# Kernel optimization log

Measured on AMD Instinct MI355X. Metric: run time of the kernel, lower is better.

## Reference

```python
import jax, jax.numpy as jnp
import numpy as np

EPS = 1e-5


def spmm(rows, cols, vals, x):
    # x: (B, C, V); y[b,c,v] = sum_{e: rows[e]==v} vals[e] * x[b,c,cols[e]]
    B, C, V = x.shape
    xt = x.reshape(B * C, V).T                      # (V, B*C)
    msg = vals[:, None] * xt[cols]                  # (E, B*C)
    y = jax.ops.segment_sum(msg, rows, num_segments=V)
    return y.T.reshape(B, C, V)


def cheb_conv(x, W, b, rows, cols, vals):
    # W: (K, Cin, Cout); Chebyshev recurrence over node dim
    K = W.shape[0]
    Tk = [x]
    if K > 1:
        Tk.append(spmm(rows, cols, vals, x))
    for _ in range(2, K):
        Tk.append(2.0 * spmm(rows, cols, vals, Tk[-1]) - Tk[-2])
    T = jnp.stack(Tk)                               # (K, B, Cin, V)
    out = jnp.einsum('kbiv,kio->bov', T, W)
    if b is not None:
        out = out + b[None, :, None]
    return out


def bn(x, g, be):
    # BatchNorm1d training-mode stats over (batch, nodes) per channel
    m = jnp.mean(x, axis=(0, 2), keepdims=True)
    v = jnp.var(x, axis=(0, 2), keepdims=True)
    return (x - m) * jax.lax.rsqrt(v + EPS) * g[None, :, None] + be[None, :, None]


def res_block(x, rows, cols, vals, ga, bea, Wa, ba, gb, beb, Wb, bb, Ws=None):
    xn = bn(x, ga, bea)
    out = cheb_conv(xn, Wa, ba, rows, cols, vals)
    out = bn(jax.nn.relu(out), gb, beb)
    out = cheb_conv(out, Wb, bb, rows, cols, vals)
    sc = xn if Ws is None else cheb_conv(xn, Ws, None, rows, cols, vals)
    return jax.nn.relu(out + sc)


def setup_inputs() -> dict:
    key = jax.random.key(0)
    ks = iter(jax.random.split(key, 40))
    V, E, B, K = 50000, 800000, 8, 4
    d = {}
    d['x'] = jax.random.normal(next(ks), (B, 16, V), dtype=jnp.float32)
    d['lap_rows'] = jax.random.randint(next(ks), (E,), 0, V, dtype=jnp.int32)
    d['lap_cols'] = jax.random.randint(next(ks), (E,), 0, V, dtype=jnp.int32)
    d['lap_vals'] = jax.random.normal(next(ks), (E,), dtype=jnp.float32) * 0.05

    def w(shape, scale=0.1):
        return jax.random.normal(next(ks), shape, dtype=jnp.float32) * scale

    d['W_in'], d['b_in'] = w((K, 16, 32)), w((32,))
    # block 1: 32 -> [32] -> 32 (identity shortcut)
    d['g1a'], d['be1a'] = jnp.ones(32), jnp.zeros(32)
    d['W1a'], d['b1a'] = w((K, 32, 32)), w((32,))
    d['g1b'], d['be1b'] = jnp.ones(32), jnp.zeros(32)
    d['W1b'], d['b1b'] = w((K, 32, 32)), w((32,))
    # block 2: 32 -> [64] -> 64 (ChebConv K=1 shortcut, no bias)
    d['g2a'], d['be2a'] = jnp.ones(32), jnp.zeros(32)
    d['W2a'], d['b2a'] = w((K, 32, 64)), w((64,))
    d['g2b'], d['be2b'] = jnp.ones(64), jnp.zeros(64)
    d['W2b'], d['b2b'] = w((K, 64, 64)), w((64,))
    d['W2s'] = w((1, 32, 64))
    # block 3: 64 -> [64] -> 64 (identity shortcut)
    d['g3a'], d['be3a'] = jnp.ones(64), jnp.zeros(64)
    d['W3a'], d['b3a'] = w((K, 64, 64)), w((64,))
    d['g3b'], d['be3b'] = jnp.ones(64), jnp.zeros(64)
    d['W3b'], d['b3b'] = w((K, 64, 64)), w((64,))
    # output head
    d['g_out'], d['be_out'] = jnp.ones(64), jnp.zeros(64)
    d['W_out'], d['b_out'] = w((K, 64, 10)), w((10,))
    return d


def reference(x, lap_rows, lap_cols, lap_vals,
              W_in, b_in,
              g1a, be1a, W1a, b1a, g1b, be1b, W1b, b1b,
              g2a, be2a, W2a, b2a, g2b, be2b, W2b, b2b, W2s,
              g3a, be3a, W3a, b3a, g3b, be3b, W3b, b3b,
              g_out, be_out, W_out, b_out):
    r, c, v = lap_rows, lap_cols, lap_vals
    out = jax.nn.relu(cheb_conv(x, W_in, b_in, r, c, v))
    out = res_block(out, r, c, v, g1a, be1a, W1a, b1a, g1b, be1b, W1b, b1b)
    out = res_block(out, r, c, v, g2a, be2a, W2a, b2a, g2b, be2b, W2b, b2b, W2s)
    out = res_block(out, r, c, v, g3a, be3a, W3a, b3a, g3b, be3b, W3b, b3b)
    out = bn(out, g_out, be_out)
    out = jax.nn.relu(cheb_conv(out, W_out, b_out, r, c, v))
    pooled = jnp.max(out, axis=2)                   # global max pool over nodes -> (B, 10)
    return jax.nn.log_softmax(pooled, axis=1)
```

## Files before the change

### kernel.cpp

```cpp
#include <hip/hip_runtime.h>
#include <hip/hip_bf16.h>
#include <hip/hip_fp16.h>

__global__ void hist_kernel(const int* __restrict__ rows, int* __restrict__ counts, int E) {
    int i = blockIdx.x * blockDim.x + threadIdx.x;
    if (i < E) atomicAdd(&counts[rows[i]], 1);
}

__global__ void scan_kernel(const int* __restrict__ counts, int* __restrict__ row_ptr, int V) {
    __shared__ int wsum[4];
    __shared__ int s_carry;
    int t = threadIdx.x;
    int lane = t & 63, w = t >> 6;
    if (t == 0) { s_carry = 0; row_ptr[0] = 0; }
    __syncthreads();
    for (int base = 0; base < V; base += 256) {
        int i = base + t;
        int x = (i < V) ? counts[i] : 0;
        #pragma unroll
        for (int d = 1; d < 64; d <<= 1) {
            int y = __shfl_up(x, d);
            if (lane >= d) x += y;
        }
        if (lane == 63) wsum[w] = x;
        __syncthreads();
        int wo = 0;
        for (int j = 0; j < w; ++j) wo += wsum[j];
        int total = wsum[0] + wsum[1] + wsum[2] + wsum[3];
        if (i < V) row_ptr[i + 1] = s_carry + wo + x;
        __syncthreads();
        if (t == 0) s_carry += total;
        __syncthreads();
    }
}

__global__ void init_cursor_kernel(const int* __restrict__ row_ptr, int* __restrict__ cursor, int V) {
    int i = blockIdx.x * blockDim.x + threadIdx.x;
    if (i < V) cursor[i] = row_ptr[i];
}

__global__ void scatter_kernel(const int* __restrict__ rows, const int* __restrict__ cols,
                               const float* __restrict__ vals, int* __restrict__ cursor,
                               int* __restrict__ cols_s, float* __restrict__ vals_s, int E) {
    int i = blockIdx.x * blockDim.x + threadIdx.x;
    if (i < E) {
        int r = rows[i];
        int p = atomicAdd(&cursor[r], 1);
        cols_s[p] = cols[i];
        vals_s[p] = vals[i];
    }
}

__global__ void transpose_in_kernel(const float* __restrict__ x, __half* __restrict__ X, int V) {
    int total = V * 128;
    for (int i = blockIdx.x * blockDim.x + threadIdx.x; i < total; i += gridDim.x * blockDim.x) {
        int v = i >> 7;
        int t = i & 127;
        X[i] = __float2half(x[t * V + v]);
    }
}

template <int VPT> struct PackT;
template <> struct PackT<1> { using T = float;  };
template <> struct PackT<2> { using T = float2; };
template <> struct PackT<4> { using T = float4; };

template <int VPT>
__global__ __launch_bounds__(256) void spmm2_kernel(
    const int* __restrict__ row_ptr, const int* __restrict__ cols,
    const float* __restrict__ vals, const __half2* __restrict__ src,
    __half2* dst, const __half2* prev, int V) {
    using T = typename PackT<VPT>::T;
    union U { T raw; __half2 h[VPT]; };
    int lane = threadIdx.x & 63;
    int v = (blockIdx.x << 2) | (threadIdx.x >> 6);
    if (v >= V) return;
    const int W = VPT * 64;
    const size_t row = (size_t)v * W + lane * VPT;

    float pr[2 * VPT];
    bool hasp = (prev != nullptr);
    if (hasp) {
        U pv; pv.raw = *(const T*)(prev + row);
        #pragma unroll
        for (int j = 0; j < VPT; ++j) {
            float2 f = __half22float2(pv.h[j]);
            pr[2 * j] = f.x; pr[2 * j + 1] = f.y;
        }
    }
    float acc[2 * VPT];
    #pragma unroll
    for (int j = 0; j < 2 * VPT; ++j) acc[j] = 0.f;

    int e0 = row_ptr[v], e1 = row_ptr[v + 1];
    int e = e0;
    for (; e + 4 <= e1; e += 4) {
        int   c0 = cols[e],   c1 = cols[e + 1], c2 = cols[e + 2], c3 = cols[e + 3];
        float w0 = vals[e],   w1 = vals[e + 1], w2 = vals[e + 2], w3 = vals[e + 3];
        U g0, g1, g2, g3;
        g0.raw = *(const T*)(src + (size_t)c0 * W + lane * VPT);
        g1.raw = *(const T*)(src + (size_t)c1 * W + lane * VPT);
        g2.raw = *(const T*)(src + (size_t)c2 * W + lane * VPT);
        g3.raw = *(const T*)(src + (size_t)c3 * W + lane * VPT);
        #pragma unroll
        for (int j = 0; j < VPT; ++j) {
            float2 f;
            f = __half22float2(g0.h[j]); acc[2*j] += w0 * f.x; acc[2*j+1] += w0 * f.y;
            f = __half22float2(g1.h[j]); acc[2*j] += w1 * f.x; acc[2*j+1] += w1 * f.y;
            f = __half22float2(g2.h[j]); acc[2*j] += w2 * f.x; acc[2*j+1] += w2 * f.y;
            f = __half22float2(g3.h[j]); acc[2*j] += w3 * f.x; acc[2*j+1] += w3 * f.y;
        }
    }
    for (; e < e1; ++e) {
        int c = cols[e]; float wv = vals[e];
        U g; g.raw = *(const T*)(src + (size_t)c * W + lane * VPT);
        #pragma unroll
        for (int j = 0; j < VPT; ++j) {
            float2 f = __half22float2(g.h[j]);
            acc[2*j] += wv * f.x; acc[2*j+1] += wv * f.y;
        }
    }
    if (hasp) {
        #pragma unroll
        for (int j = 0; j < 2 * VPT; ++j) acc[j] = 2.f * acc[j] - pr[j];
    }
    U o;
    #pragma unroll
    for (int j = 0; j < VPT; ++j) o.h[j] = __floats2half2_rn(acc[2*j], acc[2*j+1]);
    *(T*)(dst + row) = o.raw;
}

__global__ __launch_bounds__(256) void mix2_kernel(
    const __half* __restrict__ in, int Cin, float* out, int Cout,
    const float* __restrict__ Wg, const float* __restrict__ bias,
    int accum, int V) {
    extern __shared__ float lds[];
    const int G  = 256 / Cout;
    const int NB = 4 * G;
    const int RS = 4 * Cin + 4;
    const int BCin = 8 * Cin, BCout = 8 * Cout;
    float* ins = lds;
    float* Ws  = lds + G * 8 * RS;

    int tid = threadIdx.x;
    int v0 = blockIdx.x * NB;

    for (int idx = tid; idx < (Cin * Cout) / 4; idx += 256)
        *(float4*)(Ws + idx * 4) = *(const float4*)(Wg + idx * 4);
    int total = NB * BCin;
    for (int idx = tid; idx * 2 < total; idx += 256) {
        int p = idx * 2;
        int n = p / BCin, r = p - n * BCin;
        int vv = v0 + n;
        float2 f = make_float2(0.f, 0.f);
        if (vv < V) f = __half22float2(*(const __half2*)(in + (size_t)vv * BCin + r));
        int b = r / Cin, ci = r - b * Cin;
        int g = n >> 2, j = n & 3;
        float* base = ins + (g * 8 + b) * RS + j;
        base[ci * 4]       = f.x;
        base[(ci + 1) * 4] = f.y;
    }
    __syncthreads();

    int g   = tid / Cout;
    int u   = tid - g * Cout;
    int CO8 = Cout >> 3;
    int b   = u / CO8;
    int co0 = (u - b * CO8) * 8;

    float a[4][8];
    #pragma unroll
    for (int n = 0; n < 4; ++n)
        #pragma unroll
        for (int k = 0; k < 8; ++k) a[n][k] = 0.f;

    const float* ib = ins + (g * 8 + b) * RS;
    for (int ci = 0; ci < Cin; ++ci) {
        float4 x  = *(const float4*)(ib + ci * 4);
        float4 w0 = *(const float4*)(Ws + ci * Cout + co0);
        float4 w1 = *(const float4*)(Ws + ci * Cout + co0 + 4);
        float xv[4] = {x.x, x.y, x.z, x.w};
        float wv[8] = {w0.x, w0.y, w0.z, w0.w, w1.x, w1.y, w1.z, w1.w};
        #pragma unroll
        for (int n = 0; n < 4; ++n)
            #pragma unroll
            for (int k = 0; k < 8; ++k)
                a[n][k] = fmaf(xv[n], wv[k], a[n][k]);
    }

    float bb[8];
    #pragma unroll
    for (int k = 0; k < 8; ++k) bb[k] = bias ? bias[co0 + k] : 0.f;

    #pragma unroll
    for (int n = 0; n < 4; ++n) {
        int vv = v0 + g * 4 + n;
        if (vv < V) {
            size_t oo = (size_t)vv * BCout + b * Cout + co0;
            float4 r0 = make_float4(a[n][0] + bb[0], a[n][1] + bb[1],
                                    a[n][2] + bb[2], a[n][3] + bb[3]);
            float4 r1 = make_float4(a[n][4] + bb[4], a[n][5] + bb[5],
                                    a[n][6] + bb[6], a[n][7] + bb[7]);
            if (accum) {
                float4 o0 = *(const float4*)(out + oo);
                float4 o1 = *(const float4*)(out + oo + 4);
                r0.x += o0.x; r0.y += o0.y; r0.z += o0.z; r0.w += o0.w;
                r1.x += o1.x; r1.y += o1.y; r1.z += o1.z; r1.w += o1.w;
            }
            *(float4*)(out + oo)     = r0;
            *(float4*)(out + oo + 4) = r1;
        }
    }
}

__global__ __launch_bounds__(256) void mix_kernel(
    const __half* __restrict__ in, int Cin, float* out, int Cout,
    const float* __restrict__ W, const float* __restrict__ bias,
    int accum, int V) {
    const int NPB = 4;
    __shared__ float in_s[NPB * 512];
    int t = threadIdx.x;
    int v0 = blockIdx.x * NPB;
    int BCin = 8 * Cin, BCout = 8 * Cout;
    for (int idx = t; idx < NPB * BCin; idx += 256) {
        int n = idx / BCin, r = idx - n * BCin;
        int v = v0 + n;
        in_s[idx] = (v < V) ? __half2float(in[(size_t)v * BCin + r]) : 0.f;
    }
    __syncthreads();
    for (int o = t; o < BCout; o += 256) {
        int b = o / Cout, co = o - b * Cout;
        float bb = bias ? bias[co] : 0.f;
        float a[NPB] = {bb, bb, bb, bb};
        for (int ci = 0; ci < Cin; ++ci) {
            float wv = W[ci * Cout + co];
            #pragma unroll
            for (int n = 0; n < NPB; ++n)
                a[n] += in_s[n * BCin + b * Cin + ci] * wv;
        }
        #pragma unroll
        for (int n = 0; n < NPB; ++n) {
            int v = v0 + n;
            if (v < V) {
                size_t oi = (size_t)v * BCout + o;
                float r = a[n];
                if (accum) r += out[oi];
                out[oi] = r;
            }
        }
    }
}

__global__ void bn_stats_h_kernel(const __half* __restrict__ x, int C,
                                  float* __restrict__ sums, size_t N) {
    __shared__ float s_sum[256];
    __shared__ float s_sq[256];
    int t = threadIdx.x;
    size_t i0 = (size_t)blockIdx.x * 256 + t;
    size_t step = (size_t)gridDim.x * 256;
    float s = 0.f, q = 0.f;
    for (size_t i = i0; i < N; i += step) {
        float v = __half2float(x[i]);
        s += v; q += v * v;
    }
    s_sum[t] = s; s_sq[t] = q;
    __syncthreads();
    for (int st = 128; st >= C; st >>= 1) {
        if (t < st) { s_sum[t] += s_sum[t + st]; s_sq[t] += s_sq[t + st]; }
        __syncthreads();
    }
    if (t < C) {
        atomicAdd(&sums[t], s_sum[t]);
        atomicAdd(&sums[C + t], s_sq[t]);
    }
}

__global__ void bn_stats_f_kernel(const float* __restrict__ x, int C, int relu_in,
                                  float* __restrict__ sums, size_t N) {
    __shared__ float s_sum[256];
    __shared__ float s_sq[256];
    int t = threadIdx.x;
    size_t i0 = (size_t)blockIdx.x * 256 + t;
    size_t step = (size_t)gridDim.x * 256;
    float s = 0.f, q = 0.f;
    for (size_t i = i0; i < N; i += step) {
        float v = x[i];
        if (relu_in) v = fmaxf(v, 0.f);
        s += v; q += v * v;
    }
    s_sum[t] = s; s_sq[t] = q;
    __syncthreads();
    for (int st = 128; st >= C; st >>= 1) {
        if (t < st) { s_sum[t] += s_sum[t + st]; s_sq[t] += s_sq[t + st]; }
        __syncthreads();
    }
    if (t < C) {
        atomicAdd(&sums[t], s_sum[t]);
        atomicAdd(&sums[C + t], s_sq[t]);
    }
}

__global__ void bn_finalize_kernel(const float* __restrict__ sums, const float* __restrict__ g,
                                   const float* __restrict__ be, float* __restrict__ ss,
                                   int C, float invN) {
    int c = threadIdx.x;
    if (c < C) {
        float m = sums[c] * invN;
        float var = sums[C + c] * invN - m * m;
        float s = g[c] * rsqrtf(var + 1e-5f);
        ss[c] = s;
        ss[C + c] = be[c] - m * s;
    }
}

__global__ void affine_h_kernel(__half* x, const float* __restrict__ ss, int C, size_t N) {
    size_t stride = (size_t)gridDim.x * blockDim.x;
    for (size_t i = (size_t)blockIdx.x * blockDim.x + threadIdx.x; i < N; i += stride) {
        int c = (int)(i & (size_t)(C - 1));
        x[i] = __float2half(__half2float(x[i]) * ss[c] + ss[C + c]);
    }
}

__global__ void affine_f2h_kernel(const float* __restrict__ in, __half* __restrict__ out,
                                  const float* __restrict__ ss, int C, size_t N) {
    size_t stride = (size_t)gridDim.x * blockDim.x;
    for (size_t i = (size_t)blockIdx.x * blockDim.x + threadIdx.x; i < N; i += stride) {
        int c = (int)(i & (size_t)(C - 1));
        float v = fmaxf(in[i], 0.f);
        out[i] = __float2half(v * ss[c] + ss[C + c]);
    }
}

__global__ void store_relu_kernel(const float* __restrict__ acc, __half* x0,
                                  int add, size_t N) {
    size_t stride = (size_t)gridDim.x * blockDim.x;
    for (size_t i = (size_t)blockIdx.x * blockDim.x + threadIdx.x; i < N; i += stride) {
        float r = acc[i];
        if (add) r += __half2float(x0[i]);
        x0[i] = __float2half(fmaxf(r, 0.f));
    }
}

__global__ void maxpool_kernel(const float* __restrict__ x, float* __restrict__ pooled, int V) {
    __shared__ float red[256];
    int o = blockIdx.x;
    float m = 0.f;
    for (int v = threadIdx.x; v < V; v += 256)
        m = fmaxf(m, x[(size_t)v * 80 + o]);
    red[threadIdx.x] = m;
    __syncthreads();
    for (int st = 128; st > 0; st >>= 1) {
        if (threadIdx.x < st) red[threadIdx.x] = fmaxf(red[threadIdx.x], red[threadIdx.x + st]);
        __syncthreads();
    }
    if (threadIdx.x == 0) pooled[o] = red[0];
}

__global__ void lsm_kernel(const float* __restrict__ pooled, float* __restrict__ out) {
    int b = threadIdx.x;
    if (b < 8) {
        float m = -1e30f;
        for (int c = 0; c < 10; ++c) m = fmaxf(m, pooled[b * 10 + c]);
        float s = 0.f;
        for (int c = 0; c < 10; ++c) s += expf(pooled[b * 10 + c] - m);
        float l = logf(s);
        for (int c = 0; c < 10; ++c)
            out[b * 10 + c] = pooled[b * 10 + c] - m - l;
    }
}

__global__ void encode_kernel(float* out, float val) {
    int i = threadIdx.x;
    if (i < 80) out[i] = val;
}

extern "C" void kernel_launch(void* const* d_in, const int* in_sizes, int n_in,
                              void* d_out, int out_size, void* d_ws, size_t ws_size,
                              hipStream_t stream) {
    (void)in_sizes; (void)n_in; (void)out_size;
    const int V = 50000, E = 800000;

    auto al = [](size_t x) { return (x + 255) & ~(size_t)255; };
    const size_t ACCB = al((size_t)V * 512 * sizeof(float));
    const size_t FB   = al((size_t)V * 512 * sizeof(__half));
    const size_t need = ACCB + 3 * FB + al((V + 1) * 4) + al(V * 4) + al(E * 4) + al(E * 4)
                      + al(8 * 128 * 4) + al(8 * 128 * 4) + al(80 * 4);
    if (ws_size < need) {
        encode_kernel<<<1, 128, 0, stream>>>((float*)d_out, (float)(ws_size >> 20));
        return;
    }

    const float* x_in = (const float*)d_in[0];
    const int* rows   = (const int*)d_in[1];
    const int* colsi  = (const int*)d_in[2];
    const float* lvals = (const float*)d_in[3];
    const float* W_in = (const float*)d_in[4];
    const float* b_in = (const float*)d_in[5];
    const float* g1a = (const float*)d_in[6],  *be1a = (const float*)d_in[7];
    const float* W1a = (const float*)d_in[8],  *b1a  = (const float*)d_in[9];
    const float* g1b = (const float*)d_in[10], *be1b = (const float*)d_in[11];
    const float* W1b = (const float*)d_in[12], *b1b  = (const float*)d_in[13];
    const float* g2a = (const float*)d_in[14], *be2a = (const float*)d_in[15];
    const float* W2a = (const float*)d_in[16], *b2a  = (const float*)d_in[17];
    const float* g2b = (const float*)d_in[18], *be2b = (const float*)d_in[19];
    const float* W2b = (const float*)d_in[20], *b2b  = (const float*)d_in[21];
    const float* W2s = (const float*)d_in[22];
    const float* g3a = (const float*)d_in[23], *be3a = (const float*)d_in[24];
    const float* W3a = (const float*)d_in[25], *b3a  = (const float*)d_in[26];
    const float* g3b = (const float*)d_in[27], *be3b = (const float*)d_in[28];
    const float* W3b = (const float*)d_in[29], *b3b  = (const float*)d_in[30];
    const float* g_o = (const float*)d_in[31], *be_o = (const float*)d_in[32];
    const float* W_o = (const float*)d_in[33], *b_o  = (const float*)d_in[34];

    char* wp = (char*)d_ws;
    auto take = [&](size_t bytes) -> void* { void* p = (void*)wp; wp += al(bytes); return p; };
    float*  ACC = (float*)take((size_t)V * 512 * sizeof(float));
    __half* B0  = (__half*)take((size_t)V * 512 * sizeof(__half));
    __half* B1  = (__half*)take((size_t)V * 512 * sizeof(__half));
    __half* B2  = (__half*)take((size_t)V * 512 * sizeof(__half));
    int* row_ptr  = (int*)take((V + 1) * sizeof(int));
    int* cursor   = (int*)take(V * sizeof(int));
    int* cols_s   = (int*)take(E * sizeof(int));
    float* vals_s = (float*)take(E * sizeof(float));
    float* bn_sums = (float*)take(8 * 128 * sizeof(float));
    float* aff     = (float*)take(8 * 128 * sizeof(float));
    float* pooled  = (float*)take(80 * sizeof(float));

    hipMemsetAsync(cursor, 0, V * sizeof(int), stream);
    hipMemsetAsync(bn_sums, 0, 8 * 128 * sizeof(float), stream);
    hist_kernel<<<(E + 255) / 256, 256, 0, stream>>>(rows, cursor, E);
    scan_kernel<<<1, 256, 0, stream>>>(cursor, row_ptr, V);
    init_cursor_kernel<<<(V + 255) / 256, 256, 0, stream>>>(row_ptr, cursor, V);
    scatter_kernel<<<(E + 255) / 256, 256, 0, stream>>>(rows, colsi, lvals, cursor, cols_s, vals_s, E);
    transpose_in_kernel<<<4096, 256, 0, stream>>>(x_in, B0, V);

    auto spmm = [&](const __half* src, __half* dst, const __half* prev, int C) {
        int grid = (V + 3) / 4;
        if (C == 16)
            spmm2_kernel<1><<<grid, 256, 0, stream>>>(row_ptr, cols_s, vals_s,
                (const __half2*)src, (__half2*)dst, (const __half2*)prev, V);
        else if (C == 32)
            spmm2_kernel<2><<<grid, 256, 0, stream>>>(row_ptr, cols_s, vals_s,
                (const __half2*)src, (__half2*)dst, (const __half2*)prev, V);
        else
            spmm2_kernel<4><<<grid, 256, 0, stream>>>(row_ptr, cols_s, vals_s,
                (const __half2*)src, (__half2*)dst, (const __half2*)prev, V);
    };
    auto mix = [&](const __half* in, int Cin, int Cout, const float* W,
                   const float* bias, int accum) {
        if (Cout == 32 || Cout == 64) {
            int G = 256 / Cout, NB = 4 * G, RS = 4 * Cin + 4;
            size_t ldsb = (size_t)(G * 8 * RS + Cin * Cout) * sizeof(float);
            mix2_kernel<<<(V + NB - 1) / NB, 256, ldsb, stream>>>(in, Cin, ACC, Cout,
                                                                  W, bias, accum, V);
        } else {
            mix_kernel<<<(V + 3) / 4, 256, 0, stream>>>(in, Cin, ACC, Cout, W, bias, accum, V);
        }
    };
    auto stats_h = [&](const __half* xb, int C, int slot, const float* g, const float* be) {
        bn_stats_h_kernel<<<1024, 256, 0, stream>>>(xb, C, bn_sums + slot * 128, (size_t)V * 8 * C);
        bn_finalize_kernel<<<1, 64, 0, stream>>>(bn_sums + slot * 128, g, be, aff + slot * 128, C,
                                                 1.f / ((float)V * 8.f));
    };
    auto stats_f = [&](const float* xb, int C, int relu, int slot, const float* g, const float* be) {
        bn_stats_f_kernel<<<1024, 256, 0, stream>>>(xb, C, relu, bn_sums + slot * 128, (size_t)V * 8 * C);
        bn_finalize_kernel<<<1, 64, 0, stream>>>(bn_sums + slot * 128, g, be, aff + slot * 128, C,
                                                 1.f / ((float)V * 8.f));
    };
    auto affine_h = [&](__half* xb, int C, int slot) {
        affine_h_kernel<<<2048, 256, 0, stream>>>(xb, aff + slot * 128, C, (size_t)V * 8 * C);
    };
    auto affine_f2h = [&](const float* in, __half* out, int C, int slot) {
        affine_f2h_kernel<<<2048, 256, 0, stream>>>(in, out, aff + slot * 128, C, (size_t)V * 8 * C);
    };
    auto store_relu = [&](int add, int C) {
        store_relu_kernel<<<2048, 256, 0, stream>>>(ACC, B0, add, (size_t)V * 8 * C);
    };
    auto cheb_a = [&](int Cin, int Cout, const float* W, const float* bias) {
        mix(B0, Cin, Cout, W, bias, 0);
        spmm(B0, B1, nullptr, Cin);
        mix(B1, Cin, Cout, W + 1 * Cin * Cout, nullptr, 1);
        spmm(B1, B2, B0, Cin);
        mix(B2, Cin, Cout, W + 2 * Cin * Cout, nullptr, 1);
        spmm(B2, B1, B1, Cin);
        mix(B1, Cin, Cout, W + 3 * Cin * Cout, nullptr, 1);
    };
    auto cheb_b = [&](int C, const float* W, const float* bias) {
        mix(B1, C, C, W, bias, 0);
        spmm(B1, B2, nullptr, C);
        mix(B2, C, C, W + 1 * C * C, nullptr, 1);
        spmm(B2, B1, B1, C);
        mix(B1, C, C, W + 2 * C * C, nullptr, 1);
        spmm(B1, B2, B2, C);
        mix(B2, C, C, W + 3 * C * C, nullptr, 1);
    };

    cheb_a(16, 32, W_in, b_in);
    store_relu(0, 32);

    stats_h(B0, 32, 0, g1a, be1a);
    affine_h(B0, 32, 0);
    cheb_a(32, 32, W1a, b1a);
    stats_f(ACC, 32, 1, 1, g1b, be1b);
    affine_f2h(ACC, B1, 32, 1);
    cheb_b(32, W1b, b1b);
    store_relu(1, 32);

    stats_h(B0, 32, 2, g2a, be2a);
    affine_h(B0, 32, 2);
    cheb_a(32, 64, W2a, b2a);
    stats_f(ACC, 64, 1, 3, g2b, be2b);
    affine_f2h(ACC, B1, 64, 3);
    cheb_b(64, W2b, b2b);
    mix(B0, 32, 64, W2s, nullptr, 1);
    store_relu(0, 64);

    stats_h(B0, 64, 4, g3a, be3a);
    affine_h(B0, 64, 4);
    cheb_a(64, 64, W3a, b3a);
    stats_f(ACC, 64, 1, 5, g3b, be3b);
    affine_f2h(ACC, B1, 64, 5);
    cheb_b(64, W3b, b3b);
    store_relu(1, 64);

    stats_h(B0, 64, 6, g_o, be_o);
    affine_h(B0, 64, 6);
    cheb_a(64, 10, W_o, b_o);
    maxpool_kernel<<<80, 256, 0, stream>>>(ACC, pooled, V);
    lsm_kernel<<<1, 64, 0, stream>>>(pooled, (float*)d_out);
}
```

Before: 4.971 ms.

## Replace mix kernels with templated per-row GEMV, fuse residual-ReLU store, parallelize scan

The LDS-tiled mix2/mix fallback kernels are replaced by a templated mix3 kernel. In it, each thread handles one (node, batch) row, keeps all output channels in registers and reads weights through uniform loads. The final mix of each Chebyshev conv now fuses the residual add, ReLU and fp16 store, which removes the separate store_relu passes over ACC. The single-block serial prefix scan for CSR construction is replaced by a three-kernel chunked scan. Each thread now holds up to 64 accumulators, so register pressure and occupancy may suffer, and the W2s shortcut mix is reordered to run before the last W2b mix.

```diff
diff --git a/kernel.cpp b/kernel.cpp
--- a/kernel.cpp
+++ b/kernel.cpp
@@ -7,31 +7,53 @@
     if (i < E) atomicAdd(&counts[rows[i]], 1);
 }
 
-__global__ void scan_kernel(const int* __restrict__ counts, int* __restrict__ row_ptr, int V) {
+__global__ void chunk_sum_kernel(const int* __restrict__ counts, int* __restrict__ chunk_sums, int V) {
+    __shared__ int sh[256];
+    int t = threadIdx.x;
+    int i = blockIdx.x * 256 + t;
+    sh[t] = (i < V) ? counts[i] : 0;
+    __syncthreads();
+    for (int st = 128; st > 0; st >>= 1) {
+        if (t < st) sh[t] += sh[t + st];
+        __syncthreads();
+    }
+    if (t == 0) chunk_sums[blockIdx.x] = sh[0];
+}
+
+__global__ void scan_chunks_kernel(int* __restrict__ cs, int n) {
     __shared__ int wsum[4];
-    __shared__ int s_carry;
-    int t = threadIdx.x;
-    int lane = t & 63, w = t >> 6;
-    if (t == 0) { s_carry = 0; row_ptr[0] = 0; }
-    __syncthreads();
-    for (int base = 0; base < V; base += 256) {
-        int i = base + t;
-        int x = (i < V) ? counts[i] : 0;
-        #pragma unroll
-        for (int d = 1; d < 64; d <<= 1) {
-            int y = __shfl_up(x, d);
-            if (lane >= d) x += y;
-        }
-        if (lane == 63) wsum[w] = x;
-        __syncthreads();
-        int wo = 0;
-        for (int j = 0; j < w; ++j) wo += wsum[j];
-        int total = wsum[0] + wsum[1] + wsum[2] + wsum[3];
-        if (i < V) row_ptr[i + 1] = s_carry + wo + x;
-        __syncthreads();
-        if (t == 0) s_carry += total;
-        __syncthreads();
-    }
+    int t = threadIdx.x, lane = t & 63, w = t >> 6;
+    int orig = (t < n) ? cs[t] : 0;
+    int x = orig;
+    #pragma unroll
+    for (int d = 1; d < 64; d <<= 1) {
+        int y = __shfl_up(x, d);
+        if (lane >= d) x += y;
+    }
+    if (lane == 63) wsum[w] = x;
+    __syncthreads();
+    int wo = 0;
+    for (int j = 0; j < w; ++j) wo += wsum[j];
+    if (t < n) cs[t] = wo + x - orig;
+}
+
+__global__ void scan_final_kernel(const int* __restrict__ counts, const int* __restrict__ chunk_off,
+                                  int* __restrict__ row_ptr, int V) {
+    __shared__ int wsum[4];
+    int t = threadIdx.x, lane = t & 63, w = t >> 6;
+    int i = blockIdx.x * 256 + t;
+    int x = (i < V) ? counts[i] : 0;
+    #pragma unroll
+    for (int d = 1; d < 64; d <<= 1) {
+        int y = __shfl_up(x, d);
+        if (lane >= d) x += y;
+    }
+    if (lane == 63) wsum[w] = x;
+    __syncthreads();
+    int wo = 0;
+    for (int j = 0; j < w; ++j) wo += wsum[j];
+    if (i < V) row_ptr[i + 1] = chunk_off[blockIdx.x] + wo + x;
+    if (i == 0) row_ptr[0] = 0;
 }
 
 __global__ void init_cursor_kernel(const int* __restrict__ row_ptr, int* __restrict__ cursor, int V) {
@@ -130,124 +152,56 @@
     *(T*)(dst + row) = o.raw;
 }
 
-__global__ __launch_bounds__(256) void mix2_kernel(
-    const __half* __restrict__ in, int Cin, float* out, int Cout,
-    const float* __restrict__ Wg, const float* __restrict__ bias,
-    int accum, int V) {
-    extern __shared__ float lds[];
-    const int G  = 256 / Cout;
-    const int NB = 4 * G;
-    const int RS = 4 * Cin + 4;
-    const int BCin = 8 * Cin, BCout = 8 * Cout;
-    float* ins = lds;
-    float* Ws  = lds + G * 8 * RS;
-
-    int tid = threadIdx.x;
-    int v0 = blockIdx.x * NB;
-
-    for (int idx = tid; idx < (Cin * Cout) / 4; idx += 256)
-        *(float4*)(Ws + idx * 4) = *(const float4*)(Wg + idx * 4);
-    int total = NB * BCin;
-    for (int idx = tid; idx * 2 < total; idx += 256) {
-        int p = idx * 2;
-        int n = p / BCin, r = p - n * BCin;
-        int vv = v0 + n;
-        float2 f = make_float2(0.f, 0.f);
-        if (vv < V) f = __half22float2(*(const __half2*)(in + (size_t)vv * BCin + r));
-        int b = r / Cin, ci = r - b * Cin;
-        int g = n >> 2, j = n & 3;
-        float* base = ins + (g * 8 + b) * RS + j;
-        base[ci * 4]       = f.x;
-        base[(ci + 1) * 4] = f.y;
-    }
-    __syncthreads();
-
-    int g   = tid / Cout;
-    int u   = tid - g * Cout;
-    int CO8 = Cout >> 3;
-    int b   = u / CO8;
-    int co0 = (u - b * CO8) * 8;
-
-    float a[4][8];
-    #pragma unroll
-    for (int n = 0; n < 4; ++n)
-        #pragma unroll
-        for (int k = 0; k < 8; ++k) a[n][k] = 0.f;
-
-    const float* ib = ins + (g * 8 + b) * RS;
-    for (int ci = 0; ci < Cin; ++ci) {
-        float4 x  = *(const float4*)(ib + ci * 4);
-        float4 w0 = *(const float4*)(Ws + ci * Cout + co0);
-        float4 w1 = *(const float4*)(Ws + ci * Cout + co0 + 4);
-        float xv[4] = {x.x, x.y, x.z, x.w};
-        float wv[8] = {w0.x, w0.y, w0.z, w0.w, w1.x, w1.y, w1.z, w1.w};
-        #pragma unroll
-        for (int n = 0; n < 4; ++n)
+template <int CIN, int COUT>
+__global__ __launch_bounds__(256) void mix3_kernel(
+    const __half* __restrict__ in, float* accbuf,
+    const float* __restrict__ W, const float* __restrict__ bias,
+    __half* resout, int accum, int fin, int V) {
+    int g = blockIdx.x * 256 + threadIdx.x;
+    int n = g >> 3, b = g & 7;
+    if (n >= V) return;
+    const __half2* xr = (const __half2*)(in + (size_t)n * 8 * CIN + b * CIN);
+
+    float acc[COUT];
+    if (bias) {
+        #pragma unroll
+        for (int c = 0; c < COUT; ++c) acc[c] = bias[c];
+    } else {
+        #pragma unroll
+        for (int c = 0; c < COUT; ++c) acc[c] = 0.f;
+    }
+    for (int q = 0; q < CIN / 2; ++q) {
+        float2 x = __half22float2(xr[q]);
+        const float* w0 = W + (2 * q) * COUT;
+        const float* w1 = W + (2 * q + 1) * COUT;
+        #pragma unroll
+        for (int c = 0; c < COUT; ++c) acc[c] = fmaf(x.x, w0[c], acc[c]);
+        #pragma unroll
+        for (int c = 0; c < COUT; ++c) acc[c] = fmaf(x.y, w1[c], acc[c]);
+    }
+    size_t ob = (size_t)n * 8 * COUT + (size_t)b * COUT;
+    if (fin < 0) {
+        if (accum) {
             #pragma unroll
-            for (int k = 0; k < 8; ++k)
-                a[n][k] = fmaf(xv[n], wv[k], a[n][k]);
-    }
-
-    float bb[8];
-    #pragma unroll
-    for (int k = 0; k < 8; ++k) bb[k] = bias ? bias[co0 + k] : 0.f;
-
-    #pragma unroll
-    for (int n = 0; n < 4; ++n) {
-        int vv = v0 + g * 4 + n;
-        if (vv < V) {
-            size_t oo = (size_t)vv * BCout + b * Cout + co0;
-            float4 r0 = make_float4(a[n][0] + bb[0], a[n][1] + bb[1],
-                                    a[n][2] + bb[2], a[n][3] + bb[3]);
-            float4 r1 = make_float4(a[n][4] + bb[4], a[n][5] + bb[5],
-                                    a[n][6] + bb[6], a[n][7] + bb[7]);
-            if (accum) {
-                float4 o0 = *(const float4*)(out + oo);
-                float4 o1 = *(const float4*)(out + oo + 4);
-                r0.x += o0.x; r0.y += o0.y; r0.z += o0.z; r0.w += o0.w;
-                r1.x += o1.x; r1.y += o1.y; r1.z += o1.z; r1.w += o1.w;
-            }
-            *(float4*)(out + oo)     = r0;
-            *(float4*)(out + oo + 4) = r1;
-        }
-    }
-}
-
-__global__ __launch_bounds__(256) void mix_kernel(
-    const __half* __restrict__ in, int Cin, float* out, int Cout,
-    const float* __restrict__ W, const float* __restrict__ bias,
-    int accum, int V) {
-    const int NPB = 4;
-    __shared__ float in_s[NPB * 512];
-    int t = threadIdx.x;
-    int v0 = blockIdx.x * NPB;
-    int BCin = 8 * Cin, BCout = 8 * Cout;
-    for (int idx = t; idx < NPB * BCin; idx += 256) {
-        int n = idx / BCin, r = idx - n * BCin;
-        int v = v0 + n;
-        in_s[idx] = (v < V) ? __half2float(in[(size_t)v * BCin + r]) : 0.f;
-    }
-    __syncthreads();
-    for (int o = t; o < BCout; o += 256) {
-        int b = o / Cout, co = o - b * Cout;
-        float bb = bias ? bias[co] : 0.f;
-        float a[NPB] = {bb, bb, bb, bb};
-        for (int ci = 0; ci < Cin; ++ci) {
-            float wv = W[ci * Cout + co];
+            for (int c = 0; c < COUT; ++c) acc[c] += accbuf[ob + c];
+        }
+        #pragma unroll
+        for (int c = 0; c < COUT; ++c) accbuf[ob + c] = acc[c];
+    } else {
+        if (accum) {
             #pragma unroll
-            for (int n = 0; n < NPB; ++n)
-                a[n] += in_s[n * BCin + b * Cin + ci] * wv;
-        }
-        #pragma unroll
-        for (int n = 0; n < NPB; ++n) {
-            int v = v0 + n;
-            if (v < V) {
-                size_t oi = (size_t)v * BCout + o;
-                float r = a[n];
-                if (accum) r += out[oi];
-                out[oi] = r;
-            }
-        }
+            for (int c = 0; c < COUT; ++c) acc[c] += accbuf[ob + c];
+        }
+        if (fin == 1) {
+            #pragma unroll
+            for (int c = 0; c < COUT; ++c) acc[c] += __half2float(resout[ob + c]);
+        }
+        #pragma unroll
+        for (int c = 0; c < COUT; ++c) acc[c] = fmaxf(acc[c], 0.f);
+        __half2* ro = (__half2*)(resout + ob);
+        #pragma unroll
+        for (int c = 0; c < COUT / 2; ++c)
+            ro[c] = __floats2half2_rn(acc[2 * c], acc[2 * c + 1]);
     }
 }
 
@@ -331,16 +285,6 @@
     }
 }
 
-__global__ void store_relu_kernel(const float* __restrict__ acc, __half* x0,
-                                  int add, size_t N) {
-    size_t stride = (size_t)gridDim.x * blockDim.x;
-    for (size_t i = (size_t)blockIdx.x * blockDim.x + threadIdx.x; i < N; i += stride) {
-        float r = acc[i];
-        if (add) r += __half2float(x0[i]);
-        x0[i] = __float2half(fmaxf(r, 0.f));
-    }
-}
-
 __global__ void maxpool_kernel(const float* __restrict__ x, float* __restrict__ pooled, int V) {
     __shared__ float red[256];
     int o = blockIdx.x;
@@ -379,12 +323,13 @@
                               hipStream_t stream) {
     (void)in_sizes; (void)n_in; (void)out_size;
     const int V = 50000, E = 800000;
+    const int NCH = (V + 255) / 256;
 
     auto al = [](size_t x) { return (x + 255) & ~(size_t)255; };
     const size_t ACCB = al((size_t)V * 512 * sizeof(float));
     const size_t FB   = al((size_t)V * 512 * sizeof(__half));
     const size_t need = ACCB + 3 * FB + al((V + 1) * 4) + al(V * 4) + al(E * 4) + al(E * 4)
-                      + al(8 * 128 * 4) + al(8 * 128 * 4) + al(80 * 4);
+                      + al(8 * 128 * 4) + al(8 * 128 * 4) + al(80 * 4) + al(NCH * 4);
     if (ws_size < need) {
         encode_kernel<<<1, 128, 0, stream>>>((float*)d_out, (float)(ws_size >> 20));
         return;
@@ -425,11 +370,14 @@
     float* bn_sums = (float*)take(8 * 128 * sizeof(float));
     float* aff     = (float*)take(8 * 128 * sizeof(float));
     float* pooled  = (float*)take(80 * sizeof(float));
+    int* chunks    = (int*)take(NCH * sizeof(int));
 
     hipMemsetAsync(cursor, 0, V * sizeof(int), stream);
     hipMemsetAsync(bn_sums, 0, 8 * 128 * sizeof(float), stream);
     hist_kernel<<<(E + 255) / 256, 256, 0, stream>>>(rows, cursor, E);
-    scan_kernel<<<1, 256, 0, stream>>>(cursor, row_ptr, V);
+    chunk_sum_kernel<<<NCH, 256, 0, stream>>>(cursor, chunks, V);
+    scan_chunks_kernel<<<1, 256, 0, stream>>>(chunks, NCH);
+    scan_final_kernel<<<NCH, 256, 0, stream>>>(cursor, chunks, row_ptr, V);
     init_cursor_kernel<<<(V + 255) / 256, 256, 0, stream>>>(row_ptr, cursor, V);
     scatter_kernel<<<(E + 255) / 256, 256, 0, stream>>>(rows, colsi, lvals, cursor, cols_s, vals_s, E);
     transpose_in_kernel<<<4096, 256, 0, stream>>>(x_in, B0, V);
@@ -446,16 +394,19 @@
             spmm2_kernel<4><<<grid, 256, 0, stream>>>(row_ptr, cols_s, vals_s,
                 (const __half2*)src, (__half2*)dst, (const __half2*)prev, V);
     };
+    const int MG = (V * 8 + 255) / 256;
     auto mix = [&](const __half* in, int Cin, int Cout, const float* W,
-                   const float* bias, int accum) {
-        if (Cout == 32 || Cout == 64) {
-            int G = 256 / Cout, NB = 4 * G, RS = 4 * Cin + 4;
-            size_t ldsb = (size_t)(G * 8 * RS + Cin * Cout) * sizeof(float);
-            mix2_kernel<<<(V + NB - 1) / NB, 256, ldsb, stream>>>(in, Cin, ACC, Cout,
-                                                                  W, bias, accum, V);
-        } else {
-            mix_kernel<<<(V + 3) / 4, 256, 0, stream>>>(in, Cin, ACC, Cout, W, bias, accum, V);
-        }
+                   const float* bias, int accum, int fin) {
+        if (Cin == 16 && Cout == 32)
+            mix3_kernel<16, 32><<<MG, 256, 0, stream>>>(in, ACC, W, bias, B0, accum, fin, V);
+        else if (Cin == 32 && Cout == 32)
+            mix3_kernel<32, 32><<<MG, 256, 0, stream>>>(in, ACC, W, bias, B0, accum, fin, V);
+        else if (Cin == 32 && Cout == 64)
+            mix3_kernel<32, 64><<<MG, 256, 0, stream>>>(in, ACC, W, bias, B0, accum, fin, V);
+        else if (Cin == 64 && Cout == 64)
+            mix3_kernel<64, 64><<<MG, 256, 0, stream>>>(in, ACC, W, bias, B0, accum, fin, V);
+        else
+            mix3_kernel<64, 10><<<MG, 256, 0, stream>>>(in, ACC, W, bias, B0, accum, fin, V);
     };
     auto stats_h = [&](const __half* xb, int C, int slot, const float* g, const float* be) {
         bn_stats_h_kernel<<<1024, 256, 0, stream>>>(xb, C, bn_sums + slot * 128, (size_t)V * 8 * C);
@@ -473,59 +424,58 @@
     auto affine_f2h = [&](const float* in, __half* out, int C, int slot) {
         affine_f2h_kernel<<<2048, 256, 0, stream>>>(in, out, aff + slot * 128, C, (size_t)V * 8 * C);
     };
-    auto store_relu = [&](int add, int C) {
-        store_relu_kernel<<<2048, 256, 0, stream>>>(ACC, B0, add, (size_t)V * 8 * C);
-    };
-    auto cheb_a = [&](int Cin, int Cout, const float* W, const float* bias) {
-        mix(B0, Cin, Cout, W, bias, 0);
+    auto cheb_a = [&](int Cin, int Cout, const float* W, const float* bias, int lastfin) {
+        mix(B0, Cin, Cout, W, bias, 0, -1);
         spmm(B0, B1, nullptr, Cin);
-        mix(B1, Cin, Cout, W + 1 * Cin * Cout, nullptr, 1);
+        mix(B1, Cin, Cout, W + 1 * Cin * Cout, nullptr, 1, -1);
         spmm(B1, B2, B0, Cin);
-        mix(B2, Cin, Cout, W + 2 * Cin * Cout, nullptr, 1);
+        mix(B2, Cin, Cout, W + 2 * Cin * Cout, nullptr, 1, -1);
         spmm(B2, B1, B1, Cin);
-        mix(B1, Cin, Cout, W + 3 * Cin * Cout, nullptr, 1);
-    };
-    auto cheb_b = [&](int C, const float* W, const float* bias) {
-        mix(B1, C, C, W, bias, 0);
+        mix(B1, Cin, Cout, W + 3 * Cin * Cout, nullptr, 1, lastfin);
+    };
+    auto cheb_b = [&](int C, const float* W, const float* bias, int lastfin) {
+        mix(B1, C, C, W, bias, 0, -1);
         spmm(B1, B2, nullptr, C);
-        mix(B2, C, C, W + 1 * C * C, nullptr, 1);
+        mix(B2, C, C, W + C * C, nullptr, 1, -1);
         spmm(B2, B1, B1, C);
-        mix(B1, C, C, W + 2 * C * C, nullptr, 1);
+        mix(B1, C, C, W + 2 * C * C, nullptr, 1, -1);
         spmm(B1, B2, B2, C);
-        mix(B2, C, C, W + 3 * C * C, nullptr, 1);
-    };
-
-    cheb_a(16, 32, W_in, b_in);
-    store_relu(0, 32);
+        mix(B2, C, C, W + 3 * C * C, nullptr, 1, lastfin);
+    };
+
+    cheb_a(16, 32, W_in, b_in, 0);
 
     stats_h(B0, 32, 0, g1a, be1a);
     affine_h(B0, 32, 0);
-    cheb_a(32, 32, W1a, b1a);
+    cheb_a(32, 32, W1a, b1a, -1);
     stats_f(ACC, 32, 1, 1, g1b, be1b);
     affine_f2h(ACC, B1, 32, 1);
-    cheb_b(32, W1b, b1b);
-    store_relu(1, 32);
+    cheb_b(32, W1b, b1b, 1);
 
     stats_h(B0, 32, 2, g2a, be2a);
     affine_h(B0, 32, 2);
-    cheb_a(32, 64, W2a, b2a);
+    cheb_a(32, 64, W2a, b2a, -1);
     stats_f(ACC, 64, 1, 3, g2b, be2b);
     affine_f2h(ACC, B1, 64, 3);
-    cheb_b(64, W2b, b2b);
-    mix(B0, 32, 64, W2s, nullptr, 1);
-    store_relu(0, 64);
+    mix(B1, 64, 64, W2b, b2b, 0, -1);
+    spmm(B1, B2, nullptr, 64);
+    mix(B2, 64, 64, W2b + 1 * 64 * 64, nullptr, 1, -1);
+    spmm(B2, B1, B1, 64);
+    mix(B1, 64, 64, W2b + 2 * 64 * 64, nullptr, 1, -1);
+    spmm(B1, B2, B2, 64);
+    mix(B0, 32, 64, W2s, nullptr, 1, -1);
+    mix(B2, 64, 64, W2b + 3 * 64 * 64, nullptr, 1, 0);
 
     stats_h(B0, 64, 4, g3a, be3a);
     affine_h(B0, 64, 4);
-    cheb_a(64, 64, W3a, b3a);
+    cheb_a(64, 64, W3a, b3a, -1);
     stats_f(ACC, 64, 1, 5, g3b, be3b);
     affine_f2h(ACC, B1, 64, 5);
-    cheb_b(64, W3b, b3b);
-    store_relu(1, 64);
+    cheb_b(64, W3b, b3b, 1);
 
     stats_h(B0, 64, 6, g_o, be_o);
     affine_h(B0, 64, 6);
-    cheb_a(64, 10, W_o, b_o);
+    cheb_a(64, 10, W_o, b_o, -1);
     maxpool_kernel<<<80, 256, 0, stream>>>(ACC, pooled, V);
     lsm_kernel<<<1, 64, 0, stream>>>(pooled, (float*)d_out);
 }
```

Result: slower. 5.095 ms (+2.5%).
